# Kernel tuning notes

Measured on AMD Instinct MI355X. Metric: run time of the kernel, lower is better.

The kernel has to match this reference:

```python
import jax, jax.numpy as jnp
import numpy as np

# segment-boundary byte set (matches ByteContextEncoder.SEGMENT_BYTES)
_SEG_BYTES = b' \t\n\r.,;:!?()[]{}"\'' + b'+-*/=<>|&^~%@#$\\'
_SEP_TABLE = np.zeros(256, dtype=bool)
_SEP_TABLE[list(_SEG_BYTES)] = True

B, T, D, H, L = 4, 2048, 512, 8, 4
HID = 4 * D          # SwiGLU hidden dim
DH = D // H          # head dim
EPS = 1e-6
ALPHA = 0.5
ROPE_BASE = 10000.0


def setup_inputs() -> dict:
    key = jax.random.key(0)
    ks = jax.random.split(key, 10)
    std = D ** -0.5
    tokens = jax.random.randint(ks[0], (B, T), 0, 256)
    embed = jax.random.normal(ks[1], (256, D), dtype=jnp.float32) * std
    wq = jax.random.normal(ks[2], (L, D, D), dtype=jnp.float32) * std
    wk = jax.random.normal(ks[3], (L, D, D), dtype=jnp.float32) * std
    wv = jax.random.normal(ks[4], (L, D, D), dtype=jnp.float32) * std
    wo = jax.random.normal(ks[5], (L, D, D), dtype=jnp.float32) * std
    w1 = jax.random.normal(ks[6], (L, HID, D), dtype=jnp.float32) * std  # gate proj
    w3 = jax.random.normal(ks[7], (L, HID, D), dtype=jnp.float32) * std  # up proj
    w2 = jax.random.normal(ks[8], (L, D, HID), dtype=jnp.float32) * (HID ** -0.5)  # down proj
    attn_norm_w = jnp.ones((L, D), dtype=jnp.float32)
    ffn_norm_w = jnp.ones((L, D), dtype=jnp.float32)
    final_norm_w = jnp.ones((D,), dtype=jnp.float32)
    return {"tokens": tokens, "embed": embed, "attn_norm_w": attn_norm_w,
            "wq": wq, "wk": wk, "wv": wv, "wo": wo,
            "ffn_norm_w": ffn_norm_w, "w1": w1, "w2": w2, "w3": w3,
            "final_norm_w": final_norm_w}


def _rmsnorm(x, w):
    return x * jax.lax.rsqrt(jnp.mean(x * x, axis=-1, keepdims=True) + EPS) * w


def _rope_tables():
    inv = 1.0 / (ROPE_BASE ** (jnp.arange(0, DH, 2, dtype=jnp.float32) / DH))  # (DH/2,)
    ang = jnp.arange(T, dtype=jnp.float32)[:, None] * inv[None, :]             # (T, DH/2)
    return jnp.cos(ang), jnp.sin(ang)


def _apply_rope(x, cos, sin):
    # x: (B, T, H, DH); rotate interleaved pairs
    x1, x2 = x[..., ::2], x[..., 1::2]
    c = cos[None, :, None, :]
    s = sin[None, :, None, :]
    r1 = x1 * c - x2 * s
    r2 = x1 * s + x2 * c
    return jnp.stack([r1, r2], axis=-1).reshape(x.shape)


def _attention(x, Wq, Wk, Wv, Wo, cos, sin):
    q = (x @ Wq.T).reshape(B, T, H, DH)
    k = (x @ Wk.T).reshape(B, T, H, DH)
    v = (x @ Wv.T).reshape(B, T, H, DH)
    q = _apply_rope(q, cos, sin)
    k = _apply_rope(k, cos, sin)
    scores = jnp.einsum('bthd,bshd->bhts', q, k) / jnp.sqrt(jnp.float32(DH))
    a = jax.nn.softmax(scores, axis=-1)  # bidirectional (causal=False)
    o = jnp.einsum('bhts,bshd->bthd', a, v).reshape(B, T, D)
    return o @ Wo.T


def _swiglu(x, W1, W2, W3):
    return (jax.nn.silu(x @ W1.T) * (x @ W3.T)) @ W2.T


def _segment_pool(h, tokens):
    # segment ids via cumsum of separator indicator; per-batch offset b*(T+1)
    sep = jnp.asarray(_SEP_TABLE)[tokens].astype(jnp.int32)          # (B, T)
    seg = jnp.cumsum(sep, axis=1) + jnp.arange(B, dtype=jnp.int32)[:, None] * (T + 1)
    flat_s = seg.reshape(B * T)
    flat_h = h.reshape(B * T, D)
    nseg = B * (T + 1)
    seg_sum = jax.ops.segment_sum(flat_h, flat_s, num_segments=nseg)  # (nseg, D)
    seg_cnt = jax.ops.segment_sum(jnp.ones((B * T,), h.dtype), flat_s, num_segments=nseg)
    seg_cnt = jnp.maximum(seg_cnt, 1.0)
    seg_mean = (seg_sum / seg_cnt[:, None])[flat_s].reshape(B, T, D)
    return ALPHA * h + (1.0 - ALPHA) * seg_mean


def reference(tokens, embed, attn_norm_w, wq, wk, wv, wo, ffn_norm_w, w1, w2, w3, final_norm_w):
    tokens = jnp.clip(tokens, 0, 255)
    x = embed[tokens]  # (B, T, D); dropout=0 -> identity
    cos, sin = _rope_tables()
    for l in range(L):
        x = x + _attention(_rmsnorm(x, attn_norm_w[l]), wq[l], wk[l], wv[l], wo[l], cos, sin)
        x = x + _swiglu(_rmsnorm(x, ffn_norm_w[l]), w1[l], w2[l], w3[l])
    x = _rmsnorm(x, final_norm_w)
    return _segment_pool(x, tokens)
```

## Files before the change

kernel.cpp:

```cpp
#include <hip/hip_runtime.h>
#include <math.h>

#define Bq 4
#define Tt 2048
#define Dd 512
#define Hh 8
#define Ll 4
#define HIDN 2048
#define DHd 64
#define BT (Bq*Tt)
#define BTD ((size_t)BT*Dd)

typedef __attribute__((ext_vector_type(8))) __bf16 bf16x8;
typedef __attribute__((ext_vector_type(4))) __bf16 bf16x4;
typedef __attribute__((ext_vector_type(2))) __bf16 bf16x2;
typedef __attribute__((ext_vector_type(4))) float f32x4;

static __device__ __forceinline__ int is_sep(int t) {
    const unsigned long long w0 = 0xFC00FFFF00002600ULL;
    const unsigned long long w1 = 0x7800000078000001ULL;
    if (t < 64)  return (int)((w0 >> t) & 1ULL);
    if (t < 128) return (int)((w1 >> (t - 64)) & 1ULL);
    return 0;
}

static __device__ __forceinline__ void gload16(const void* g, void* l) {
    __builtin_amdgcn_global_load_lds(
        (const __attribute__((address_space(1))) void*)g,
        (__attribute__((address_space(3))) void*)l, 16, 0, 0);
}

__global__ void embed_kernel(const int* __restrict__ tokens, const float* __restrict__ embed,
                             float* __restrict__ x) {
    size_t idx = (size_t)blockIdx.x * blockDim.x + threadIdx.x;
    if (idx >= BTD / 4) return;
    size_t row = idx >> 7;
    int tk = tokens[row];
    tk = tk < 0 ? 0 : (tk > 255 ? 255 : tk);
    const float4* src = (const float4*)(embed + (size_t)tk * Dd);
    ((float4*)x)[idx] = src[idx & 127];
}

__global__ void rope_table_kernel(float* __restrict__ cosb, float* __restrict__ sinb) {
    int idx = blockIdx.x * blockDim.x + threadIdx.x;
    if (idx >= Tt * 32) return;
    int t = idx >> 5, j = idx & 31;
    float inv = powf(10000.0f, -(2.0f * j) / 64.0f);
    float ang = (float)t * inv;
    cosb[idx] = cosf(ang);
    sinb[idx] = sinf(ang);
}

__global__ void cvt_bf16_kernel(const float* __restrict__ in, __bf16* __restrict__ out, int n8) {
    int i = blockIdx.x * blockDim.x + threadIdx.x;
    if (i >= n8) return;
    const float4* p = (const float4*)(in + (size_t)i * 8);
    float4 a = p[0], b = p[1];
    bf16x8 o8;
    o8[0] = (__bf16)a.x; o8[1] = (__bf16)a.y; o8[2] = (__bf16)a.z; o8[3] = (__bf16)a.w;
    o8[4] = (__bf16)b.x; o8[5] = (__bf16)b.y; o8[6] = (__bf16)b.z; o8[7] = (__bf16)b.w;
    *(bf16x8*)(out + (size_t)i * 8) = o8;
}

__global__ void cvt_qkv_kernel(const float* __restrict__ wq, const float* __restrict__ wk,
                               const float* __restrict__ wv, __bf16* __restrict__ out) {
    int i = blockIdx.x * blockDim.x + threadIdx.x;
    if (i >= 393216) return;
    int l = i / 98304;
    int r = i - l * 98304;
    int t = r >> 15;
    int pos8 = r & 32767;
    const float* src = (t == 0 ? wq : (t == 1 ? wk : wv)) + (size_t)l * 262144 + (size_t)pos8 * 8;
    float4 a = *(const float4*)src;
    float4 b = *(const float4*)(src + 4);
    bf16x8 o8;
    o8[0] = (__bf16)a.x; o8[1] = (__bf16)a.y; o8[2] = (__bf16)a.z; o8[3] = (__bf16)a.w;
    o8[4] = (__bf16)b.x; o8[5] = (__bf16)b.y; o8[6] = (__bf16)b.z; o8[7] = (__bf16)b.w;
    *(bf16x8*)(out + (size_t)i * 8) = o8;
}

__global__ void rmsnorm_kernel(const float* __restrict__ x, const float* __restrict__ w,
                               float* __restrict__ y) {
    int row = blockIdx.x;
    int tid = threadIdx.x;
    const float2* xr = (const float2*)(x + (size_t)row * Dd);
    float2 v = xr[tid];
    __shared__ float red[256];
    red[tid] = v.x * v.x + v.y * v.y;
    __syncthreads();
    for (int off = 128; off > 0; off >>= 1) {
        if (tid < off) red[tid] += red[tid + off];
        __syncthreads();
    }
    float scale = rsqrtf(red[0] * (1.0f / Dd) + 1e-6f);
    float2 wv = ((const float2*)w)[tid];
    ((float2*)(y + (size_t)row * Dd))[tid] = make_float2(v.x * scale * wv.x, v.y * scale * wv.y);
}

__global__ void rmsnorm_bf16_kernel(const float* __restrict__ x, const float* __restrict__ w,
                                    __bf16* __restrict__ y) {
    int row = blockIdx.x;
    int tid = threadIdx.x;
    const float2* xr = (const float2*)(x + (size_t)row * Dd);
    float2 v = xr[tid];
    __shared__ float red[256];
    red[tid] = v.x * v.x + v.y * v.y;
    __syncthreads();
    for (int off = 128; off > 0; off >>= 1) {
        if (tid < off) red[tid] += red[tid + off];
        __syncthreads();
    }
    float scale = rsqrtf(red[0] * (1.0f / Dd) + 1e-6f);
    float2 wv = ((const float2*)w)[tid];
    bf16x2 o;
    o[0] = (__bf16)(v.x * scale * wv.x);
    o[1] = (__bf16)(v.y * scale * wv.y);
    *(bf16x2*)(y + (size_t)row * Dd + 2 * tid) = o;
}

template<int EPI>
__global__ __launch_bounds__(256) void gemm_bt_mfma(
    const __bf16* __restrict__ A, const __bf16* __restrict__ Bw,
    const float* __restrict__ res, void* __restrict__ Cout,
    int N, int K,
    const float* __restrict__ cosb, const float* __restrict__ sinb) {
    __shared__ __align__(16) __bf16 lds[2][2][128 * 32];
    const int tid = threadIdx.x;
    const int w = tid >> 6, lane = tid & 63;
    const int l15 = lane & 15, g4 = lane >> 4;
    const int wr = w >> 1, wc = w & 1;
    const int bm = blockIdx.y * 128, bn = blockIdx.x * 128;
    const int lrow = lane >> 2, lc8 = (lane & 3) * 8;
    const int chunk0 = w * 2;

    f32x4 acc[4][4];
    #pragma unroll
    for (int m = 0; m < 4; m++)
        #pragma unroll
        for (int n = 0; n < 4; n++) acc[m][n] = (f32x4){0.f, 0.f, 0.f, 0.f};

    auto stage = [&](int buf, int k0) {
        #pragma unroll
        for (int c = 0; c < 2; c++) {
            int chunk = chunk0 + c;
            const __bf16* ga = A + (size_t)(bm + chunk * 16 + lrow) * K + k0 + lc8;
            gload16(ga, &lds[buf][0][chunk * 512]);
            const __bf16* gb = Bw + (size_t)(bn + chunk * 16 + lrow) * K + k0 + lc8;
            gload16(gb, &lds[buf][1][chunk * 512]);
        }
    };

    stage(0, 0);
    __syncthreads();
    const int NT = K >> 5;
    int cur = 0;
    for (int t = 0; t < NT; t++) {
        if (t + 1 < NT) stage(cur ^ 1, (t + 1) << 5);
        const __bf16* Al = &lds[cur][0][0];
        const __bf16* Bl = &lds[cur][1][0];
        bf16x8 af[4], bfr[4];
        #pragma unroll
        for (int m = 0; m < 4; m++)
            af[m] = *(const bf16x8*)&Al[(wr * 64 + m * 16 + l15) * 32 + g4 * 8];
        #pragma unroll
        for (int n = 0; n < 4; n++)
            bfr[n] = *(const bf16x8*)&Bl[(wc * 64 + n * 16 + l15) * 32 + g4 * 8];
        #pragma unroll
        for (int m = 0; m < 4; m++)
            #pragma unroll
            for (int n = 0; n < 4; n++)
                acc[m][n] = __builtin_amdgcn_mfma_f32_16x16x32_bf16(af[m], bfr[n], acc[m][n], 0, 0, 0);
        __syncthreads();
        cur ^= 1;
    }

    #pragma unroll
    for (int m = 0; m < 4; m++)
        #pragma unroll
        for (int n = 0; n < 4; n++)
            #pragma unroll
            for (int r = 0; r < 4; r++) {
                size_t row = bm + wr * 64 + m * 16 + g4 * 4 + r;
                int col = bn + wc * 64 + n * 16 + l15;
                if (EPI == 0) {
                    ((__bf16*)Cout)[row * N + col] = (__bf16)acc[m][n][r];
                } else if (EPI == 1) {
                    ((float*)Cout)[row * N + col] = acc[m][n][r] + res[row * N + col];
                } else {
                    float vv = acc[m][n][r];
                    float vp = __shfl_xor(vv, 1);
                    if (col < 1024) {
                        int trow = (int)(row & (Tt - 1));
                        int p = (col & 63) >> 1;
                        float c = cosb[trow * 32 + p];
                        float s = sinb[trow * 32 + p];
                        float x1 = (col & 1) ? vp : vv;
                        float x2 = (col & 1) ? vv : vp;
                        float rot = (col & 1) ? (x1 * s + x2 * c) : (x1 * c - x2 * s);
                        if (col < 512) rot *= 0.18033688011112043f;
                        vv = rot;
                    }
                    ((__bf16*)Cout)[(size_t)(col >> 9) * BTD + row * 512 + (col & 511)] =
                        (__bf16)vv;
                }
            }
}

__global__ __launch_bounds__(256) void gemm_bt_mfma64(
    const __bf16* __restrict__ A, const __bf16* __restrict__ Bw,
    const float* __restrict__ res, float* __restrict__ Cout,
    int N, int K) {
    __shared__ __align__(16) __bf16 lds[2][2][64 * 32];
    const int tid = threadIdx.x;
    const int w = tid >> 6, lane = tid & 63;
    const int l15 = lane & 15, g4 = lane >> 4;
    const int wr = w >> 1, wc = w & 1;
    const int bm = blockIdx.y * 64, bn = blockIdx.x * 64;
    const int srow = tid >> 2, scol8 = (tid & 3) * 8;

    f32x4 acc[2][2];
    #pragma unroll
    for (int m = 0; m < 2; m++)
        #pragma unroll
        for (int n = 0; n < 2; n++) acc[m][n] = (f32x4){0.f, 0.f, 0.f, 0.f};

    auto stage = [&](int buf, int k0) {
        gload16(A + (size_t)(bm + srow) * K + k0 + scol8, &lds[buf][0][srow * 32 + scol8]);
        gload16(Bw + (size_t)(bn + srow) * K + k0 + scol8, &lds[buf][1][srow * 32 + scol8]);
    };

    stage(0, 0);
    __syncthreads();
    const int NT = K >> 5;
    int cur = 0;
    for (int t = 0; t < NT; t++) {
        if (t + 1 < NT) stage(cur ^ 1, (t + 1) << 5);
        const __bf16* Al = &lds[cur][0][0];
        const __bf16* Bl = &lds[cur][1][0];
        bf16x8 af[2], bfr[2];
        #pragma unroll
        for (int m = 0; m < 2; m++)
            af[m] = *(const bf16x8*)&Al[(wr * 32 + m * 16 + l15) * 32 + g4 * 8];
        #pragma unroll
        for (int n = 0; n < 2; n++)
            bfr[n] = *(const bf16x8*)&Bl[(wc * 32 + n * 16 + l15) * 32 + g4 * 8];
        #pragma unroll
        for (int m = 0; m < 2; m++)
            #pragma unroll
            for (int n = 0; n < 2; n++)
                acc[m][n] = __builtin_amdgcn_mfma_f32_16x16x32_bf16(af[m], bfr[n], acc[m][n], 0, 0, 0);
        __syncthreads();
        cur ^= 1;
    }

    #pragma unroll
    for (int m = 0; m < 2; m++)
        #pragma unroll
        for (int n = 0; n < 2; n++)
            #pragma unroll
            for (int r = 0; r < 4; r++) {
                size_t row = bm + wr * 32 + m * 16 + g4 * 4 + r;
                int col = bn + wc * 32 + n * 16 + l15;
                Cout[row * N + col] = acc[m][n][r] + res[row * N + col];
            }
}

__global__ __launch_bounds__(256) void gemm_swiglu_mfma(
    const __bf16* __restrict__ A, const __bf16* __restrict__ W1,
    const __bf16* __restrict__ W3, __bf16* __restrict__ G,
    int N, int K) {
    __shared__ __align__(16) __bf16 lds[2][3][128 * 32];
    const int tid = threadIdx.x;
    const int w = tid >> 6, lane = tid & 63;
    const int l15 = lane & 15, g4 = lane >> 4;
    const int wr = w >> 1, wc = w & 1;
    const int bm = blockIdx.y * 128, bn = blockIdx.x * 128;
    const int lrow = lane >> 2, lc8 = (lane & 3) * 8;
    const int chunk0 = w * 2;

    f32x4 acc1[4][4], acc3[4][4];
    #pragma unroll
    for (int m = 0; m < 4; m++)
        #pragma unroll
        for (int n = 0; n < 4; n++) {
            acc1[m][n] = (f32x4){0.f, 0.f, 0.f, 0.f};
            acc3[m][n] = (f32x4){0.f, 0.f, 0.f, 0.f};
        }

    auto stage = [&](int buf, int k0) {
        #pragma unroll
        for (int c = 0; c < 2; c++) {
            int chunk = chunk0 + c;
            const __bf16* ga = A + (size_t)(bm + chunk * 16 + lrow) * K + k0 + lc8;
            gload16(ga, &lds[buf][0][chunk * 512]);
            const __bf16* g1 = W1 + (size_t)(bn + chunk * 16 + lrow) * K + k0 + lc8;
            gload16(g1, &lds[buf][1][chunk * 512]);
            const __bf16* g3 = W3 + (size_t)(bn + chunk * 16 + lrow) * K + k0 + lc8;
            gload16(g3, &lds[buf][2][chunk * 512]);
        }
    };

    stage(0, 0);
    __syncthreads();
    const int NT = K >> 5;
    int cur = 0;
    for (int t = 0; t < NT; t++) {
        if (t + 1 < NT) stage(cur ^ 1, (t + 1) << 5);
        const __bf16* Al = &lds[cur][0][0];
        const __bf16* B1 = &lds[cur][1][0];
        const __bf16* B3 = &lds[cur][2][0];
        bf16x8 af[4];
        #pragma unroll
        for (int m = 0; m < 4; m++)
            af[m] = *(const bf16x8*)&Al[(wr * 64 + m * 16 + l15) * 32 + g4 * 8];
        #pragma unroll
        for (int n = 0; n < 4; n++) {
            bf16x8 b1 = *(const bf16x8*)&B1[(wc * 64 + n * 16 + l15) * 32 + g4 * 8];
            bf16x8 b3 = *(const bf16x8*)&B3[(wc * 64 + n * 16 + l15) * 32 + g4 * 8];
            #pragma unroll
            for (int m = 0; m < 4; m++) {
                acc1[m][n] = __builtin_amdgcn_mfma_f32_16x16x32_bf16(af[m], b1, acc1[m][n], 0, 0, 0);
                acc3[m][n] = __builtin_amdgcn_mfma_f32_16x16x32_bf16(af[m], b3, acc3[m][n], 0, 0, 0);
            }
        }
        __syncthreads();
        cur ^= 1;
    }

    #pragma unroll
    for (int m = 0; m < 4; m++)
        #pragma unroll
        for (int n = 0; n < 4; n++)
            #pragma unroll
            for (int r = 0; r < 4; r++) {
                size_t row = bm + wr * 64 + m * 16 + g4 * 4 + r;
                size_t col = bn + wc * 64 + n * 16 + l15;
                float a1 = acc1[m][n][r];
                float sig = 1.0f / (1.0f + __expf(-a1));
                G[row * N + col] = (__bf16)(a1 * sig * acc3[m][n][r]);
            }
}

__global__ __launch_bounds__(256) void attn_mfma_kernel(
    const __bf16* __restrict__ q, const __bf16* __restrict__ k,
    const __bf16* __restrict__ v, __bf16* __restrict__ o) {
    __shared__ __align__(16) __bf16 Ks[64][72];
    __shared__ __align__(16) __bf16 Vt[64][68];
    __shared__ __align__(16) __bf16 Ps[4][16][72];

    int tid = threadIdx.x;
    int w = tid >> 6;
    int lane = tid & 63;
    int l15 = lane & 15;
    int g = lane >> 4;
    int bh = blockIdx.y;
    int b = bh >> 3, h = bh & 7;
    int qbase = blockIdx.x * 64;

    const __bf16* qp = q + (size_t)b * Tt * Dd + (size_t)h * DHd;
    const __bf16* kp = k + (size_t)b * Tt * Dd + (size_t)h * DHd;
    const __bf16* vp = v + (size_t)b * Tt * Dd + (size_t)h * DHd;

    int r2 = tid >> 3;
    int sc8 = (tid & 7) * 8;

    bf16x8 qa[2];
    {
        const __bf16* qrow = qp + (size_t)(qbase + w * 16 + l15) * Dd;
        qa[0] = *(const bf16x8*)(qrow + g * 8);
        qa[1] = *(const bf16x8*)(qrow + 32 + g * 8);
    }

    f32x4 oacc[4];
    #pragma unroll
    for (int i = 0; i < 4; i++) oacc[i] = (f32x4){0.f, 0.f, 0.f, 0.f};
    float mrun[4] = {-1e30f, -1e30f, -1e30f, -1e30f};
    float lrun[4] = {0.f, 0.f, 0.f, 0.f};

    bf16x8 kreg[2], vreg[2];
    auto ldkv = [&](int t) {
        size_t base = (size_t)(t * 64) * Dd;
        kreg[0] = *(const bf16x8*)(kp + base + (size_t)r2 * Dd + sc8);
        kreg[1] = *(const bf16x8*)(kp + base + (size_t)(r2 + 32) * Dd + sc8);
        vreg[0] = *(const bf16x8*)(vp + base + (size_t)(2 * r2) * Dd + sc8);
        vreg[1] = *(const bf16x8*)(vp + base + (size_t)(2 * r2 + 1) * Dd + sc8);
    };

    ldkv(0);
    const int NT = Tt / 64;
    for (int t = 0; t < NT; t++) {
        __syncthreads();
        *(bf16x8*)&Ks[r2][sc8] = kreg[0];
        *(bf16x8*)&Ks[r2 + 32][sc8] = kreg[1];
        {
            const unsigned short* v0 = (const unsigned short*)&vreg[0];
            const unsigned short* v1 = (const unsigned short*)&vreg[1];
            #pragma unroll
            for (int j = 0; j < 8; j++) {
                unsigned int word = (unsigned int)v0[j] | ((unsigned int)v1[j] << 16);
                *(unsigned int*)&Vt[sc8 + j][2 * r2] = word;
            }
        }
        if (t + 1 < NT) ldkv(t + 1);
        __syncthreads();

        f32x4 s4[4];
        __builtin_amdgcn_s_setprio(1);
        #pragma unroll
        for (int c = 0; c < 4; c++) {
            s4[c] = (f32x4){0.f, 0.f, 0.f, 0.f};
            bf16x8 kb0 = *(const bf16x8*)&Ks[c * 16 + l15][g * 8];
            s4[c] = __builtin_amdgcn_mfma_f32_16x16x32_bf16(qa[0], kb0, s4[c], 0, 0, 0);
            bf16x8 kb1 = *(const bf16x8*)&Ks[c * 16 + l15][32 + g * 8];
            s4[c] = __builtin_amdgcn_mfma_f32_16x16x32_bf16(qa[1], kb1, s4[c], 0, 0, 0);
        }
        __builtin_amdgcn_s_setprio(0);

        float alpha[4];
        #pragma unroll
        for (int r = 0; r < 4; r++) {
            float tm = fmaxf(fmaxf(s4[0][r], s4[1][r]), fmaxf(s4[2][r], s4[3][r]));
            #pragma unroll
            for (int off = 1; off < 16; off <<= 1)
                tm = fmaxf(tm, __shfl_xor(tm, off));
            float mnew = fmaxf(mrun[r], tm);
            alpha[r] = exp2f(mrun[r] - mnew);
            mrun[r] = mnew;
        }
        float plane[4] = {0.f, 0.f, 0.f, 0.f};
        #pragma unroll
        for (int c = 0; c < 4; c++)
            #pragma unroll
            for (int r = 0; r < 4; r++) {
                float e = exp2f(s4[c][r] - mrun[r]);
                s4[c][r] = e;
                plane[r] += e;
            }
        #pragma unroll
        for (int r = 0; r < 4; r++)
            lrun[r] = lrun[r] * alpha[r] + plane[r];
        #pragma unroll
        for (int d2 = 0; d2 < 4; d2++)
            #pragma unroll
            for (int r = 0; r < 4; r++) oacc[d2][r] *= alpha[r];
        #pragma unroll
        for (int c = 0; c < 4; c++)
            #pragma unroll
            for (int r = 0; r < 4; r++)
                Ps[w][g * 4 + r][c * 16 + l15] = (__bf16)s4[c][r];

        bf16x8 pa0 = *(const bf16x8*)&Ps[w][l15][g * 8];
        bf16x8 pa1 = *(const bf16x8*)&Ps[w][l15][32 + g * 8];
        __builtin_amdgcn_s_setprio(1);
        #pragma unroll
        for (int d2 = 0; d2 < 4; d2++) {
            int d = d2 * 16 + l15;
            bf16x4 lo0 = *(const bf16x4*)&Vt[d][g * 8];
            bf16x4 hi0 = *(const bf16x4*)&Vt[d][g * 8 + 4];
            bf16x4 lo1 = *(const bf16x4*)&Vt[d][32 + g * 8];
            bf16x4 hi1 = *(const bf16x4*)&Vt[d][32 + g * 8 + 4];
            bf16x8 vb0, vb1;
            #pragma unroll
            for (int j = 0; j < 4; j++) {
                vb0[j] = lo0[j]; vb0[4 + j] = hi0[j];
                vb1[j] = lo1[j]; vb1[4 + j] = hi1[j];
            }
            oacc[d2] = __builtin_amdgcn_mfma_f32_16x16x32_bf16(pa0, vb0, oacc[d2], 0, 0, 0);
            oacc[d2] = __builtin_amdgcn_mfma_f32_16x16x32_bf16(pa1, vb1, oacc[d2], 0, 0, 0);
        }
        __builtin_amdgcn_s_setprio(0);
    }

    #pragma unroll
    for (int r = 0; r < 4; r++) {
        #pragma unroll
        for (int off = 1; off < 16; off <<= 1)
            lrun[r] += __shfl_xor(lrun[r], off);
    }

    __bf16* op = o + (size_t)b * Tt * Dd + (size_t)h * DHd;
    #pragma unroll
    for (int d2 = 0; d2 < 4; d2++)
        #pragma unroll
        for (int r = 0; r < 4; r++)
            op[(size_t)(qbase + w * 16 + g * 4 + r) * Dd + d2 * 16 + l15] =
                (__bf16)(oacc[d2][r] / lrun[r]);
}

__global__ void seg_scan_kernel(const int* __restrict__ tokens, int* __restrict__ segid) {
    int b = blockIdx.x;
    int tid = threadIdx.x;
    const int* trow = tokens + (size_t)b * Tt;
    int base = tid * 8;
    int inc[8];
    int run = 0;
    #pragma unroll
    for (int i = 0; i < 8; i++) {
        int tk = trow[base + i];
        tk = tk < 0 ? 0 : (tk > 255 ? 255 : tk);
        run += is_sep(tk);
        inc[i] = run;
    }
    __shared__ int part[256];
    part[tid] = run;
    __syncthreads();
    for (int off = 1; off < 256; off <<= 1) {
        int vv = (tid >= off) ? part[tid - off] : 0;
        __syncthreads();
        part[tid] += vv;
        __syncthreads();
    }
    int exc = part[tid] - run;
    #pragma unroll
    for (int i = 0; i < 8; i++)
        segid[(size_t)b * Tt + base + i] = exc + inc[i] + b * (Tt + 1);
}

__global__ void seg_cnt_kernel(const int* __restrict__ segid, float* __restrict__ cnt) {
    int i = blockIdx.x * blockDim.x + threadIdx.x;
    if (i < BT) atomicAdd(&cnt[segid[i]], 1.0f);
}

__global__ void seg_accum_kernel(const float* __restrict__ h, const int* __restrict__ segid,
                                 float* __restrict__ segsum) {
    size_t idx = (size_t)blockIdx.x * blockDim.x + threadIdx.x;
    if (idx >= BTD) return;
    size_t row = idx >> 9;
    int d = idx & 511;
    atomicAdd(&segsum[(size_t)segid[row] * Dd + d], h[idx]);
}

__global__ void seg_final_kernel(const float* __restrict__ h, const float* __restrict__ segsum,
                                 const float* __restrict__ cnt, const int* __restrict__ segid,
                                 float* __restrict__ out) {
    size_t idx = (size_t)blockIdx.x * blockDim.x + threadIdx.x;
    if (idx >= BTD) return;
    size_t row = idx >> 9;
    int d = idx & 511;
    int s = segid[row];
    float mean = segsum[(size_t)s * Dd + d] / fmaxf(cnt[s], 1.0f);
    out[idx] = 0.5f * h[idx] + 0.5f * mean;
}

extern "C" void kernel_launch(void* const* d_in, const int* in_sizes, int n_in,
                              void* d_out, int out_size, void* d_ws, size_t ws_size,
                              hipStream_t stream) {
    const int*   tokens       = (const int*)d_in[0];
    const float* embedw       = (const float*)d_in[1];
    const float* attn_norm_w  = (const float*)d_in[2];
    const float* wq           = (const float*)d_in[3];
    const float* wk           = (const float*)d_in[4];
    const float* wv           = (const float*)d_in[5];
    const float* wo           = (const float*)d_in[6];
    const float* ffn_norm_w   = (const float*)d_in[7];
    const float* w1           = (const float*)d_in[8];
    const float* w2           = (const float*)d_in[9];
    const float* w3           = (const float*)d_in[10];
    const float* final_norm_w = (const float*)d_in[11];
    float* out = (float*)d_out;
    float* ws  = (float*)d_ws;

    float*  x    = ws;
    __bf16* qkvo = (__bf16*)(ws + BTD);
    __bf16* qb   = qkvo;
    __bf16* kb   = qkvo + BTD;
    __bf16* vb   = qkvo + 2 * BTD;
    __bf16* obuf = qkvo + 3 * BTD;
    __bf16* gbuf = qkvo;
    float*  segsum = ws;
    float*  hfin   = ws + 2 * BTD;
    __bf16* xnb  = (__bf16*)(ws + 3 * BTD);
    __bf16* wb   = (__bf16*)(ws + 3 * BTD + BTD / 2);
    float*  cosb = ws + 3 * BTD + BTD / 2 + 8388608;
    float*  sinb = cosb + (size_t)Tt * 32;
    float*  segcnt = sinb + (size_t)Tt * 32;
    int*    segid  = (int*)(segcnt + Bq * (Tt + 1));

    __bf16* wqkvb = wb;
    __bf16* wob = wb + 3145728;
    __bf16* w1b = wb + 4194304;
    __bf16* w3b = wb + 8388608;
    __bf16* w2b = wb + 12582912;

    cvt_qkv_kernel<<<1536, 256, 0, stream>>>(wq, wk, wv, wqkvb);
    cvt_bf16_kernel<<<512, 256, 0, stream>>>(wo, wob, 131072);
    cvt_bf16_kernel<<<2048, 256, 0, stream>>>(w1, w1b, 524288);
    cvt_bf16_kernel<<<2048, 256, 0, stream>>>(w3, w3b, 524288);
    cvt_bf16_kernel<<<2048, 256, 0, stream>>>(w2, w2b, 524288);

    embed_kernel<<<(int)((BTD / 4 + 255) / 256), 256, 0, stream>>>(tokens, embedw, x);
    rope_table_kernel<<<(Tt * 32 + 255) / 256, 256, 0, stream>>>(cosb, sinb);

    dim3 gqkv(12, 64);
    dim3 g64(8, 128);
    dim3 gs(16, 64);
    dim3 ga(Tt / 64, Bq * Hh);

    for (int l = 0; l < Ll; l++) {
        size_t oDD = (size_t)l * Dd * Dd;
        size_t oHD = (size_t)l * HIDN * Dd;
        rmsnorm_bf16_kernel<<<BT, 256, 0, stream>>>(x, attn_norm_w + (size_t)l * Dd, xnb);
        gemm_bt_mfma<2><<<gqkv, 256, 0, stream>>>(xnb, wqkvb + (size_t)l * 786432, nullptr, qb,
                                                  1536, Dd, cosb, sinb);
        attn_mfma_kernel<<<ga, 256, 0, stream>>>(qb, kb, vb, obuf);
        gemm_bt_mfma64<<<g64, 256, 0, stream>>>(obuf, wob + oDD, x, x, Dd, Dd);
        rmsnorm_bf16_kernel<<<BT, 256, 0, stream>>>(x, ffn_norm_w + (size_t)l * Dd, xnb);
        gemm_swiglu_mfma<<<gs, 256, 0, stream>>>(xnb, w1b + oHD, w3b + oHD, gbuf, HIDN, Dd);
        gemm_bt_mfma64<<<g64, 256, 0, stream>>>(gbuf, w2b + oHD, x, x, Dd, HIDN);
    }

    rmsnorm_kernel<<<BT, 256, 0, stream>>>(x, final_norm_w, hfin);

    hipMemsetAsync(segsum, 0, (size_t)Bq * (Tt + 1) * Dd * sizeof(float), stream);
    hipMemsetAsync(segcnt, 0, (size_t)Bq * (Tt + 1) * sizeof(float), stream);
    seg_scan_kernel<<<Bq, 256, 0, stream>>>(tokens, segid);
    seg_cnt_kernel<<<(BT + 255) / 256, 256, 0, stream>>>(segid, segcnt);
    seg_accum_kernel<<<(int)((BTD + 255) / 256), 256, 0, stream>>>(hfin, segid, segsum);
    seg_final_kernel<<<(int)((BTD + 255) / 256), 256, 0, stream>>>(hfin, segsum, segcnt, segid, out);
}
```

Measured before the change: 1.195 ms.

## Split attention KV range across two blocks and merge partial softmax results

Attention blocks now each process half of the key/value tiles (grid gains a z dimension), writing unnormalized partial outputs plus running max and sum to scratch. A new merge kernel combines the two partials with softmax rescaling into the final output. This doubles block count to improve occupancy and load balance, at the cost of extra global traffic for partial results and an additional kernel launch per layer.

```diff
diff --git a/kernel.cpp b/kernel.cpp
--- a/kernel.cpp
+++ b/kernel.cpp
@@ -10,6 +10,8 @@
 #define DHd 64
 #define BT (Bq*Tt)
 #define BTD ((size_t)BT*Dd)
+#define NSPLIT 2
+#define MLSTRIDE (Bq*Hh*Tt)
 
 typedef __attribute__((ext_vector_type(8))) __bf16 bf16x8;
 typedef __attribute__((ext_vector_type(4))) __bf16 bf16x4;
@@ -343,7 +345,8 @@
 
 __global__ __launch_bounds__(256) void attn_mfma_kernel(
     const __bf16* __restrict__ q, const __bf16* __restrict__ k,
-    const __bf16* __restrict__ v, __bf16* __restrict__ o) {
+    const __bf16* __restrict__ v, __bf16* __restrict__ opart,
+    float* __restrict__ mpart, float* __restrict__ lpart) {
     __shared__ __align__(16) __bf16 Ks[64][72];
     __shared__ __align__(16) __bf16 Vt[64][68];
     __shared__ __align__(16) __bf16 Ps[4][16][72];
@@ -356,6 +359,7 @@
     int bh = blockIdx.y;
     int b = bh >> 3, h = bh & 7;
     int qbase = blockIdx.x * 64;
+    int z = blockIdx.z;
 
     const __bf16* qp = q + (size_t)b * Tt * Dd + (size_t)h * DHd;
     const __bf16* kp = k + (size_t)b * Tt * Dd + (size_t)h * DHd;
@@ -386,9 +390,10 @@
         vreg[1] = *(const bf16x8*)(vp + base + (size_t)(2 * r2 + 1) * Dd + sc8);
     };
 
-    ldkv(0);
-    const int NT = Tt / 64;
-    for (int t = 0; t < NT; t++) {
+    const int T0 = z * (Tt / 64 / NSPLIT);
+    const int NT = Tt / 64 / NSPLIT;
+    ldkv(T0);
+    for (int tt = 0; tt < NT; tt++) {
         __syncthreads();
         *(bf16x8*)&Ks[r2][sc8] = kreg[0];
         *(bf16x8*)&Ks[r2 + 32][sc8] = kreg[1];
@@ -401,7 +406,7 @@
                 *(unsigned int*)&Vt[sc8 + j][2 * r2] = word;
             }
         }
-        if (t + 1 < NT) ldkv(t + 1);
+        if (tt + 1 < NT) ldkv(T0 + tt + 1);
         __syncthreads();
 
         f32x4 s4[4];
@@ -478,13 +483,48 @@
             lrun[r] += __shfl_xor(lrun[r], off);
     }
 
-    __bf16* op = o + (size_t)b * Tt * Dd + (size_t)h * DHd;
+    __bf16* op = opart + (size_t)z * BTD + (size_t)b * Tt * Dd + (size_t)h * DHd;
     #pragma unroll
     for (int d2 = 0; d2 < 4; d2++)
         #pragma unroll
         for (int r = 0; r < 4; r++)
             op[(size_t)(qbase + w * 16 + g * 4 + r) * Dd + d2 * 16 + l15] =
-                (__bf16)(oacc[d2][r] / lrun[r]);
+                (__bf16)oacc[d2][r];
+    if (l15 == 0) {
+        int mlbase = z * MLSTRIDE + bh * Tt + qbase + w * 16 + g * 4;
+        #pragma unroll
+        for (int r = 0; r < 4; r++) {
+            mpart[mlbase + r] = mrun[r];
+            lpart[mlbase + r] = lrun[r];
+        }
+    }
+}
+
+__global__ void attn_merge_kernel(const __bf16* __restrict__ opart,
+                                  const float* __restrict__ mpart,
+                                  const float* __restrict__ lpart,
+                                  __bf16* __restrict__ o) {
+    size_t i = (size_t)blockIdx.x * blockDim.x + threadIdx.x;
+    if (i >= BTD / 8) return;
+    size_t e8 = i * 8;
+    int d = (int)(e8 & 511);
+    size_t bt = e8 >> 9;
+    int t = (int)(bt & (Tt - 1));
+    int b = (int)(bt >> 11);
+    int h = d >> 6;
+    int mlidx = (b * Hh + h) * Tt + t;
+    float m0 = mpart[mlidx], m1 = mpart[MLSTRIDE + mlidx];
+    float l0 = lpart[mlidx], l1 = lpart[MLSTRIDE + mlidx];
+    float m = fmaxf(m0, m1);
+    float w0 = exp2f(m0 - m), w1 = exp2f(m1 - m);
+    float inv = 1.0f / (w0 * l0 + w1 * l1);
+    bf16x8 a = *(const bf16x8*)(opart + e8);
+    bf16x8 c = *(const bf16x8*)(opart + BTD + e8);
+    bf16x8 r;
+    #pragma unroll
+    for (int j = 0; j < 8; j++)
+        r[j] = (__bf16)((w0 * (float)a[j] + w1 * (float)c[j]) * inv);
+    *(bf16x8*)(o + e8) = r;
 }
 
 __global__ void seg_scan_kernel(const int* __restrict__ tokens, int* __restrict__ segid) {
@@ -575,6 +615,10 @@
     float*  sinb = cosb + (size_t)Tt * 32;
     float*  segcnt = sinb + (size_t)Tt * 32;
     int*    segid  = (int*)(segcnt + Bq * (Tt + 1));
+    float*  mpart  = (float*)(segid + BT);
+    float*  lpart  = mpart + NSPLIT * MLSTRIDE;
+
+    __bf16* opart = (__bf16*)d_out;
 
     __bf16* wqkvb = wb;
     __bf16* wob = wb + 3145728;
@@ -594,7 +638,7 @@
     dim3 gqkv(12, 64);
     dim3 g64(8, 128);
     dim3 gs(16, 64);
-    dim3 ga(Tt / 64, Bq * Hh);
+    dim3 ga(Tt / 64, Bq * Hh, NSPLIT);
 
     for (int l = 0; l < Ll; l++) {
         size_t oDD = (size_t)l * Dd * Dd;
@@ -602,7 +646,8 @@
         rmsnorm_bf16_kernel<<<BT, 256, 0, stream>>>(x, attn_norm_w + (size_t)l * Dd, xnb);
         gemm_bt_mfma<2><<<gqkv, 256, 0, stream>>>(xnb, wqkvb + (size_t)l * 786432, nullptr, qb,
                                                   1536, Dd, cosb, sinb);
-        attn_mfma_kernel<<<ga, 256, 0, stream>>>(qb, kb, vb, obuf);
+        attn_mfma_kernel<<<ga, 256, 0, stream>>>(qb, kb, vb, opart, mpart, lpart);
+        attn_merge_kernel<<<(int)((BTD / 8 + 255) / 256), 256, 0, stream>>>(opart, mpart, lpart, obuf);
         gemm_bt_mfma64<<<g64, 256, 0, stream>>>(obuf, wob + oDD, x, x, Dd, Dd);
         rmsnorm_bf16_kernel<<<BT, 256, 0, stream>>>(x, ffn_norm_w + (size_t)l * Dd, xnb);
         gemm_swiglu_mfma<<<gs, 256, 0, stream>>>(xnb, w1b + oHD, w3b + oHD, gbuf, HIDN, Dd);
```

Result: no change. 1.204 ms (+0.8%).
